# Kernel optimization log

Hardware: AMD Instinct MI355X
Metric: run time of the kernel (lower is better)

Reference implementation:

```python
import jax, jax.numpy as jnp
import numpy as np

N = 20000      # nodes
E = 100000     # edges
B = 128        # graphs in batch
F_IN = 14      # node feature dim
DIM = 64       # hidden dim
E_FEAT = 4     # edge feature dim
MLP_H = 128    # edge MLP hidden


def setup_inputs() -> dict:
    key = jax.random.key(0)
    ks = jax.random.split(key, 26)

    def rn(k, shape, fan_in):
        return jax.random.normal(k, shape, jnp.float32) / np.sqrt(fan_in)

    d = {}
    d['x'] = jax.random.normal(ks[0], (N, F_IN), jnp.float32)
    d['edge_attr'] = jax.random.uniform(ks[1], (E, E_FEAT), jnp.float32)
    d['edge_index'] = jax.random.randint(ks[2], (2, E), 0, N)
    d['batch'] = jnp.sort(jax.random.randint(ks[3], (N,), 0, B))
    # lin0
    d['lin0_w'] = rn(ks[4], (F_IN, DIM), F_IN)
    d['lin0_b'] = jnp.zeros((DIM,), jnp.float32)
    # edge MLP: Linear(4,128) -> ReLU -> Linear(128, dim*dim)
    d['mlp_w1'] = rn(ks[5], (E_FEAT, MLP_H), E_FEAT)
    d['mlp_b1'] = jnp.zeros((MLP_H,), jnp.float32)
    d['mlp_w2'] = rn(ks[6], (MLP_H, DIM * DIM), MLP_H) * 0.1
    d['mlp_b2'] = jnp.zeros((DIM * DIM,), jnp.float32)
    # NNConv root weight + bias
    d['conv_root'] = rn(ks[7], (DIM, DIM), DIM)
    d['conv_bias'] = jnp.zeros((DIM,), jnp.float32)
    # GRU (input dim DIM, hidden DIM), torch gate order r,z,n
    d['gru_wi'] = rn(ks[8], (DIM, 3 * DIM), DIM)
    d['gru_wh'] = rn(ks[9], (DIM, 3 * DIM), DIM)
    d['gru_bi'] = jnp.zeros((3 * DIM,), jnp.float32)
    d['gru_bh'] = jnp.zeros((3 * DIM,), jnp.float32)
    # Set2Set LSTM (input 2*DIM, hidden DIM), torch gate order i,f,g,o
    d['lstm_wi'] = rn(ks[10], (2 * DIM, 4 * DIM), 2 * DIM)
    d['lstm_wh'] = rn(ks[11], (DIM, 4 * DIM), DIM)
    d['lstm_bi'] = jnp.zeros((4 * DIM,), jnp.float32)
    d['lstm_bh'] = jnp.zeros((4 * DIM,), jnp.float32)
    # output head
    d['lin1_w'] = rn(ks[12], (2 * DIM, DIM), 2 * DIM)
    d['lin1_b'] = jnp.zeros((DIM,), jnp.float32)
    d['lin2_w'] = rn(ks[13], (DIM, 1), DIM)
    d['lin2_b'] = jnp.zeros((1,), jnp.float32)
    return d


def _forward(x, edge_attr, edge_index, batch,
             lin0_w, lin0_b, mlp_w1, mlp_b1, mlp_w2, mlp_b2,
             conv_root, conv_bias,
             gru_wi, gru_wh, gru_bi, gru_bh,
             lstm_wi, lstm_wh, lstm_bi, lstm_bh,
             lin1_w, lin1_b, lin2_w, lin2_b):
    src, dst = edge_index[0], edge_index[1]

    out = jax.nn.relu(x @ lin0_w + lin0_b)            # [N, DIM]
    h = out                                            # GRU hidden

    # per-edge weight matrices from edge MLP (shared across the 3 steps)
    ew = jax.nn.relu(edge_attr @ mlp_w1 + mlp_b1) @ mlp_w2 + mlp_b2
    ew = ew.reshape(E, DIM, DIM)                       # [E, DIM, DIM]
    # incoming-edge counts for scatter-mean
    cnt = jax.ops.segment_sum(jnp.ones((E,), jnp.float32), dst, num_segments=N)
    cnt = jnp.maximum(cnt, 1.0)[:, None]

    for _ in range(3):
        msg = jnp.einsum('ei,eio->eo', out[src], ew)   # gather + per-edge matmul
        agg = jax.ops.segment_sum(msg, dst, num_segments=N) / cnt
        m = jax.nn.relu(agg + out @ conv_root + conv_bias)
        # GRU cell (torch gate order: r, z, n)
        gi = m @ gru_wi + gru_bi
        gh = h @ gru_wh + gru_bh
        r = jax.nn.sigmoid(gi[:, :DIM] + gh[:, :DIM])
        z = jax.nn.sigmoid(gi[:, DIM:2 * DIM] + gh[:, DIM:2 * DIM])
        n = jnp.tanh(gi[:, 2 * DIM:] + r * gh[:, 2 * DIM:])
        h = (1.0 - z) * n + z * h
        out = h

    # Set2Set pooling, 3 processing steps
    q_star = jnp.zeros((B, 2 * DIM), jnp.float32)
    hl = jnp.zeros((B, DIM), jnp.float32)
    cl = jnp.zeros((B, DIM), jnp.float32)
    for _ in range(3):
        gates = q_star @ lstm_wi + hl @ lstm_wh + lstm_bi + lstm_bh  # [B, 4*DIM]
        i = jax.nn.sigmoid(gates[:, :DIM])
        f = jax.nn.sigmoid(gates[:, DIM:2 * DIM])
        g = jnp.tanh(gates[:, 2 * DIM:3 * DIM])
        o = jax.nn.sigmoid(gates[:, 3 * DIM:])
        cl = f * cl + i * g
        hl = o * jnp.tanh(cl)
        q = hl                                         # [B, DIM]
        e = jnp.sum(out * q[batch], axis=-1)           # [N]
        emax = jax.ops.segment_max(e, batch, num_segments=B)
        emax = jnp.where(jnp.isfinite(emax), emax, 0.0)
        a = jnp.exp(e - emax[batch])
        asum = jax.ops.segment_sum(a, batch, num_segments=B)
        a = a / jnp.maximum(asum, 1e-16)[batch]
        r_vec = jax.ops.segment_sum(a[:, None] * out, batch, num_segments=B)
        q_star = jnp.concatenate([q, r_vec], axis=-1)  # [B, 2*DIM]

    y = jax.nn.relu(q_star @ lin1_w + lin1_b) @ lin2_w + lin2_b
    return y.reshape(-1)                               # [B]


def reference(x, edge_attr, edge_index, batch,
              lin0_w, lin0_b, mlp_w1, mlp_b1, mlp_w2, mlp_b2,
              conv_root, conv_bias,
              gru_wi, gru_wh, gru_bi, gru_bh,
              lstm_wi, lstm_wh, lstm_bi, lstm_bh,
              lin1_w, lin1_b, lin2_w, lin2_b):
    return _forward(x, edge_attr, edge_index, batch,
                    lin0_w, lin0_b, mlp_w1, mlp_b1, mlp_w2, mlp_b2,
                    conv_root, conv_bias,
                    gru_wi, gru_wh, gru_bi, gru_bh,
                    lstm_wi, lstm_wh, lstm_bi, lstm_bh,
                    lin1_w, lin1_b, lin2_w, lin2_b)
```

## Files before the change

### kernel.cpp

```cpp
#include <hip/hip_runtime.h>
#include <math.h>

#define N_ 20000
#define E_ 100000
#define B_ 128
#define F_IN_ 14
#define DIM_ 64
#define E_FEAT_ 4
#define MLP_H_ 128
#define EWC_ 4096
#define PC_ 8192
#define PC2_ 8256

typedef __attribute__((ext_vector_type(4))) float f32x4;
typedef __attribute__((ext_vector_type(8))) _Float16 halfx8;

__global__ void lin0_kernel(const float* __restrict__ x, const float* __restrict__ w,
                            const float* __restrict__ b, float* __restrict__ out) {
    int idx = blockIdx.x * blockDim.x + threadIdx.x;
    if (idx >= N_ * DIM_) return;
    int n = idx >> 6, d = idx & 63;
    float acc = b[d];
#pragma unroll
    for (int f = 0; f < F_IN_; ++f) acc = fmaf(x[n * F_IN_ + f], w[f * DIM_ + d], acc);
    out[idx] = acc > 0.f ? acc : 0.f;
}

__global__ void deg_boff_kernel(const int* __restrict__ src, const int* __restrict__ dst,
                                float* __restrict__ cnt, int* __restrict__ cnt_src,
                                const int* __restrict__ batch, int* __restrict__ off_b) {
    int e = blockIdx.x * blockDim.x + threadIdx.x;
    if (e < E_) {
        atomicAdd(&cnt[dst[e]], 1.0f);
        atomicAdd(&cnt_src[src[e]], 1);
    }
    if (blockIdx.x == 0 && threadIdx.x <= B_) {
        int b = threadIdx.x;
        int lo = 0, hi = N_;
        while (lo < hi) {
            int mid = (lo + hi) >> 1;
            if (batch[mid] < b) lo = mid + 1; else hi = mid;
        }
        off_b[b] = lo;
    }
}

__global__ void scan_src(const int* __restrict__ cnt_src, int* __restrict__ src_off) {
    __shared__ int part[256];
    __shared__ int off[257];
    int t = threadIdx.x;
    const int per = (N_ + 255) / 256;
    int base = t * per;
    int s = 0;
    for (int i = 0; i < per; ++i) { int b = base + i; if (b < N_) s += cnt_src[b]; }
    part[t] = s;
    __syncthreads();
    if (t == 0) {
        int a = 0;
        for (int i = 0; i < 256; ++i) { off[i] = a; a += part[i]; }
        off[256] = a;
    }
    __syncthreads();
    int run = off[t];
    for (int i = 0; i < per; ++i) {
        int b = base + i;
        if (b < N_) { src_off[b] = run; run += cnt_src[b]; }
    }
    if (t == 0) src_off[N_] = off[256];
}

__global__ __launch_bounds__(256) void scatter_mlp1(
        const int* __restrict__ src, const int* __restrict__ dst,
        int* __restrict__ cur, const int* __restrict__ src_off,
        const float* __restrict__ ea, const float* __restrict__ w1,
        const float* __restrict__ b1, int* __restrict__ dsts,
        _Float16* __restrict__ h1s) {
    __shared__ float w1s[E_FEAT_ * MLP_H_];
    __shared__ float b1s[MLP_H_];
    int t = threadIdx.x;
    if (t < MLP_H_) b1s[t] = b1[t];
    for (int i = t; i < E_FEAT_ * MLP_H_; i += 256) w1s[i] = w1[i];
    __syncthreads();
    int e = blockIdx.x * 256 + t;
    if (e >= E_) return;
    int s = src[e];
    int p = src_off[s] + atomicAdd(&cur[s], 1);
    dsts[p] = dst[e];
    float a0 = ea[e * 4 + 0], a1 = ea[e * 4 + 1];
    float a2 = ea[e * 4 + 2], a3 = ea[e * 4 + 3];
    _Float16* hrow = h1s + (size_t)p * 128;
#pragma unroll
    for (int k8 = 0; k8 < 16; ++k8) {
        halfx8 v;
#pragma unroll
        for (int j = 0; j < 8; ++j) {
            int k = k8 * 8 + j;
            float acc = b1s[k];
            acc = fmaf(a0, w1s[k], acc);
            acc = fmaf(a1, w1s[128 + k], acc);
            acc = fmaf(a2, w1s[256 + k], acc);
            acc = fmaf(a3, w1s[384 + k], acc);
            v[j] = (_Float16)(acc > 0.f ? acc : 0.f);
        }
        *(halfx8*)&hrow[k8 * 8] = v;
    }
}

__global__ void prep_b(const float* __restrict__ w2, const float* __restrict__ b2,
                       _Float16* __restrict__ Bf) {
    int idx = blockIdx.x * blockDim.x + threadIdx.x;
    if (idx >= PC2_ * 64) return;
    int c16 = idx >> 10;
    int r   = idx & 1023;
    int ks  = r >> 9;
    int q   = (r >> 7) & 3;
    int lr  = (r >> 3) & 15;
    int j   = r & 7;
    int c = c16 * 16 + lr;
    int i = ks * 32 + q * 8 + j;
    float v;
    if (c < PC_) {
        int o = c >> 7, k = c & 127;
        v = w2[(size_t)k * EWC_ + i * 64 + o];
    } else {
        int o = c - PC_;
        v = b2[i * 64 + o];
    }
    Bf[idx] = (_Float16)v;
}

__global__ __launch_bounds__(512, 4) void fused_msg(
        const float* __restrict__ out, const _Float16* __restrict__ Bf,
        const _Float16* __restrict__ h1s,
        const int* __restrict__ dsts, const int* __restrict__ src_off,
        float* __restrict__ agg) {
    __shared__ _Float16 Plds[16 * 2048];
    const int tid = threadIdx.x;
    const int lane = tid & 63;
    const int w = __builtin_amdgcn_readfirstlane(tid >> 6);
    const int lrow = lane & 15, quad = lane >> 4;
    const int nb0 = blockIdx.x * 16;

    halfx8 aG[2];
    {
        const float* orow = out + (size_t)(nb0 + lrow) * 64 + quad * 8;
#pragma unroll
        for (int ks = 0; ks < 2; ++ks) {
            float4 v0 = *(const float4*)(orow + ks * 32);
            float4 v1 = *(const float4*)(orow + ks * 32 + 4);
            aG[ks][0] = (_Float16)v0.x; aG[ks][1] = (_Float16)v0.y;
            aG[ks][2] = (_Float16)v0.z; aG[ks][3] = (_Float16)v0.w;
            aG[ks][4] = (_Float16)v1.x; aG[ks][5] = (_Float16)v1.y;
            aG[ks][6] = (_Float16)v1.z; aG[ks][7] = (_Float16)v1.w;
        }
    }

    f32x4 qf[4];
#pragma unroll
    for (int f = 0; f < 4; ++f) {
        const _Float16* bc = &Bf[(size_t)(512 + f) * 1024 + quad * 128 + lrow * 8];
        halfx8 bq0 = *(const halfx8*)bc;
        halfx8 bq1 = *(const halfx8*)(bc + 512);
        f32x4 z = (f32x4){0.f, 0.f, 0.f, 0.f};
        z = __builtin_amdgcn_mfma_f32_16x16x32_f16(aG[0], bq0, z, 0, 0, 0);
        z = __builtin_amdgcn_mfma_f32_16x16x32_f16(aG[1], bq1, z, 0, 0, 0);
        qf[f] = z;
    }

    const int n0g = nb0 + 2 * w;
    const int beg0 = src_off[n0g];
    const int end0 = src_off[n0g + 1];
    const int end1 = src_off[n0g + 2];

#pragma unroll
    for (int p = 0; p < 4; ++p) {
        if (p) __syncthreads();

#pragma unroll 8
        for (int nf = 0; nf < 16; ++nf) {
            int cl = w * 256 + nf * 16 + lrow;
            size_t tb = (size_t)(p * 128 + w * 16 + nf) * 1024 + quad * 128 + lrow * 8;
            halfx8 b0 = *(const halfx8*)&Bf[tb];
            halfx8 b1 = *(const halfx8*)&Bf[tb + 512];
            f32x4 acc = (f32x4){0.f, 0.f, 0.f, 0.f};
            acc = __builtin_amdgcn_mfma_f32_16x16x32_f16(aG[0], b0, acc, 0, 0, 0);
            acc = __builtin_amdgcn_mfma_f32_16x16x32_f16(aG[1], b1, acc, 0, 0, 0);
            int o = cl >> 7, k = cl & 127;
            int kz = k ^ (quad << 5) ^ ((o & 7) << 3);
            int base = o * 2048 + kz;
#pragma unroll
            for (int rr = 0; rr < 4; ++rr)
                Plds[base + (quad * 4 + rr) * 128] = (_Float16)acc[rr];
        }
        __syncthreads();

        int o0 = p * 16;
#pragma unroll
        for (int nn = 0; nn < 2; ++nn) {
            int nl = 2 * w + nn;
            int beg = nn ? end0 : beg0;
            int endv = nn ? end1 : end0;
            if (beg == endv) continue;
            int srcl = ((nl >> 2) << 4) | lrow;
            int rsel = nl & 3;
            float qel = rsel == 0 ? qf[p][0] : rsel == 1 ? qf[p][1]
                      : rsel == 2 ? qf[p][2] : qf[p][3];
            float qv = __shfl(qel, srcl, 64);
            halfx8 bf[4];
#pragma unroll
            for (int ks = 0; ks < 4; ++ks) {
                int kk = (ks * 32 + quad * 8) ^ ((nl >> 2) << 5) ^ ((lrow & 7) << 3);
                bf[ks] = *(const halfx8*)&Plds[lrow * 2048 + nl * 128 + kk];
            }
            for (int g = beg; g < endv; g += 16) {
                int gcnt = endv - g; if (gcnt > 16) gcnt = 16;
                int ei = lrow < gcnt ? lrow : gcnt - 1;
                int gi = g + ei;
                int dv = dsts[gi];
                halfx8 af[4];
#pragma unroll
                for (int ks = 0; ks < 4; ++ks)
                    af[ks] = *(const halfx8*)&h1s[(size_t)gi * 128 + ks * 32 + quad * 8];
                f32x4 acc = (f32x4){0.f, 0.f, 0.f, 0.f};
#pragma unroll
                for (int ks = 0; ks < 4; ++ks)
                    acc = __builtin_amdgcn_mfma_f32_16x16x32_f16(
                        af[ks], bf[ks], acc, 0, 0, 0);
#pragma unroll
                for (int rr = 0; rr < 4; ++rr) {
                    int j = quad * 4 + rr;
                    int d = __shfl(dv, j, 64);
                    if (j < gcnt) {
                        atomicAdd(&agg[(size_t)d * 64 + o0 + lrow], acc[rr] + qv);
                    }
                }
            }
        }
    }
}

__global__ __launch_bounds__(256) void gru_kernel(float* __restrict__ out,
                                                  float* __restrict__ agg,
                                                  const float* __restrict__ cnt,
                                                  const float* __restrict__ root,
                                                  const float* __restrict__ cbias,
                                                  const float* __restrict__ wi,
                                                  const float* __restrict__ wh,
                                                  const float* __restrict__ bi,
                                                  const float* __restrict__ bh) {
    __shared__ float root_s[64 * 64];
    __shared__ float h_s[32 * 64];
    __shared__ float m_s[32 * 64];
    int tid = threadIdx.x;
    int lane = tid & 63;
    int wv = __builtin_amdgcn_readfirstlane(tid >> 6);
    int nb = blockIdx.x * 32;
#pragma unroll
    for (int it = 0; it < 4; ++it) {
        int i = it * 1024 + tid * 4;
        *(float4*)&root_s[i] = *(const float4*)&root[i];
    }
#pragma unroll
    for (int it = 0; it < 2; ++it) {
        int i = it * 1024 + tid * 4;
        *(float4*)&h_s[i] = *(const float4*)&out[(size_t)nb * 64 + i];
    }
    __syncthreads();

    int nbase = nb + wv * 8;
    float a[8];
#pragma unroll
    for (int j = 0; j < 8; ++j) {
        int n = nbase + j;
        float c = cnt[n]; c = c > 1.f ? c : 1.f;
        a[j] = agg[(size_t)n * 64 + lane] / c + cbias[lane];
        agg[(size_t)n * 64 + lane] = 0.f;
    }
    for (int i = 0; i < 64; ++i) {
        float rv = root_s[i * 64 + lane];
#pragma unroll
        for (int j = 0; j < 8; ++j)
            a[j] = fmaf(h_s[(wv * 8 + j) * 64 + i], rv, a[j]);
    }
#pragma unroll
    for (int j = 0; j < 8; ++j) {
        float m = a[j] > 0.f ? a[j] : 0.f;
        m_s[(wv * 8 + j) * 64 + lane] = m;
    }
    __syncthreads();

    float gir[8], giz[8], gin[8], ghr[8], ghz[8], ghn[8];
    float bi0 = bi[lane], bi1 = bi[64 + lane], bi2 = bi[128 + lane];
    float bh0 = bh[lane], bh1 = bh[64 + lane], bh2 = bh[128 + lane];
#pragma unroll
    for (int j = 0; j < 8; ++j) {
        gir[j] = bi0; giz[j] = bi1; gin[j] = bi2;
        ghr[j] = bh0; ghz[j] = bh1; ghn[j] = bh2;
    }
    for (int i = 0; i < 64; ++i) {
        float w0 = wi[i * 192 + lane];
        float w1 = wi[i * 192 + 64 + lane];
        float w2v = wi[i * 192 + 128 + lane];
        float u0 = wh[i * 192 + lane];
        float u1 = wh[i * 192 + 64 + lane];
        float u2 = wh[i * 192 + 128 + lane];
#pragma unroll
        for (int j = 0; j < 8; ++j) {
            float mi = m_s[(wv * 8 + j) * 64 + i];
            float hi = h_s[(wv * 8 + j) * 64 + i];
            gir[j] = fmaf(mi, w0, gir[j]);
            giz[j] = fmaf(mi, w1, giz[j]);
            gin[j] = fmaf(mi, w2v, gin[j]);
            ghr[j] = fmaf(hi, u0, ghr[j]);
            ghz[j] = fmaf(hi, u1, ghz[j]);
            ghn[j] = fmaf(hi, u2, ghn[j]);
        }
    }
#pragma unroll
    for (int j = 0; j < 8; ++j) {
        int n = nbase + j;
        float rg = 1.f / (1.f + expf(-(gir[j] + ghr[j])));
        float zg = 1.f / (1.f + expf(-(giz[j] + ghz[j])));
        float ng = tanhf(gin[j] + rg * ghn[j]);
        float h = h_s[(wv * 8 + j) * 64 + lane];
        out[(size_t)n * 64 + lane] = (1.f - zg) * ng + zg * h;
    }
}

__global__ __launch_bounds__(256) void lstm_all_kernel(
        const float* __restrict__ out, const int* __restrict__ off_b,
        float* __restrict__ e_ws,
        const float* __restrict__ wi, const float* __restrict__ wh,
        const float* __restrict__ bi, const float* __restrict__ bh,
        const float* __restrict__ hw1, const float* __restrict__ hb1,
        const float* __restrict__ hw2, const float* __restrict__ hb2,
        float* __restrict__ y) {
    int b = blockIdx.x;
    int t = threadIdx.x;
    __shared__ float qs[128], hs[64], cs[64], g[256];
    __shared__ float q[64];
    __shared__ float red[256], racc[256], sasum[4];

    if (t < 128) qs[t] = 0.f;
    if (t < 64) { hs[t] = 0.f; cs[t] = 0.f; }
    __syncthreads();

    int start = off_b[b], end = off_b[b + 1];

    for (int s = 0; s < 3; ++s) {
        {
            float acc = bi[t] + bh[t];
#pragma unroll 8
            for (int i = 0; i < 128; ++i) acc = fmaf(qs[i], wi[i * 256 + t], acc);
#pragma unroll 8
            for (int i = 0; i < 64; ++i) acc = fmaf(hs[i], wh[i * 256 + t], acc);
            g[t] = acc;
        }
        __syncthreads();
        if (t < 64) {
            float ig = 1.f / (1.f + expf(-g[t]));
            float fg = 1.f / (1.f + expf(-g[64 + t]));
            float gg = tanhf(g[128 + t]);
            float og = 1.f / (1.f + expf(-g[192 + t]));
            float c = fg * cs[t] + ig * gg;
            cs[t] = c;
            float h = og * tanhf(c);
            hs[t] = h;
            q[t] = h;
        }
        __syncthreads();

        float lmax = -1e30f;
        for (int n = start + t; n < end; n += 256) {
            float acc = 0.f;
#pragma unroll 16
            for (int d2 = 0; d2 < 64; ++d2) acc = fmaf(out[n * 64 + d2], q[d2], acc);
            e_ws[n] = acc;
            lmax = fmaxf(lmax, acc);
        }
        red[t] = lmax;
        __syncthreads();
        for (int s2 = 128; s2 > 0; s2 >>= 1) {
            if (t < s2) red[t] = fmaxf(red[t], red[t + s2]);
            __syncthreads();
        }
        float emax = red[0];
        int w = t >> 6, d = t & 63;
        float rl = 0.f, lasum = 0.f;
        for (int n = start + w; n < end; n += 4) {
            float a = expf(e_ws[n] - emax);
            rl = fmaf(a, out[n * 64 + d], rl);
            if (d == 0) lasum += a;
        }
        racc[t] = rl;
        if (d == 0) sasum[w] = lasum;
        __syncthreads();
        if (t < 64) {
            float r = racc[t] + racc[64 + t] + racc[128 + t] + racc[192 + t];
            float as = sasum[0] + sasum[1] + sasum[2] + sasum[3];
            as = fmaxf(as, 1e-16f);
            qs[t] = q[t];
            qs[64 + t] = r / as;
        }
        __syncthreads();
    }

    if (t < 64) {
        float acc = hb1[t];
#pragma unroll 8
        for (int i = 0; i < 128; ++i) acc = fmaf(qs[i], hw1[i * 64 + t], acc);
        acc = acc > 0.f ? acc : 0.f;
        float p = acc * hw2[t];
        for (int off = 32; off > 0; off >>= 1) p += __shfl_down(p, off, 64);
        if (t == 0) y[b] = p + hb2[0];
    }
}

extern "C" void kernel_launch(void* const* d_in, const int* in_sizes, int n_in,
                              void* d_out, int out_size, void* d_ws, size_t ws_size,
                              hipStream_t stream) {
    (void)in_sizes; (void)n_in; (void)out_size; (void)ws_size;
    const float* x        = (const float*)d_in[0];
    const float* ea       = (const float*)d_in[1];
    const int*   eidx     = (const int*)d_in[2];
    const int*   batch    = (const int*)d_in[3];
    const float* lin0_w   = (const float*)d_in[4];
    const float* lin0_b   = (const float*)d_in[5];
    const float* mlp_w1   = (const float*)d_in[6];
    const float* mlp_b1   = (const float*)d_in[7];
    const float* mlp_w2   = (const float*)d_in[8];
    const float* mlp_b2   = (const float*)d_in[9];
    const float* conv_root= (const float*)d_in[10];
    const float* conv_bias= (const float*)d_in[11];
    const float* gru_wi   = (const float*)d_in[12];
    const float* gru_wh   = (const float*)d_in[13];
    const float* gru_bi   = (const float*)d_in[14];
    const float* gru_bh   = (const float*)d_in[15];
    const float* lstm_wi  = (const float*)d_in[16];
    const float* lstm_wh  = (const float*)d_in[17];
    const float* lstm_bi  = (const float*)d_in[18];
    const float* lstm_bh  = (const float*)d_in[19];
    const float* lin1_w   = (const float*)d_in[20];
    const float* lin1_b   = (const float*)d_in[21];
    const float* lin2_w   = (const float*)d_in[22];
    const float* lin2_b   = (const float*)d_in[23];
    float* y = (float*)d_out;

    const int* src = eidx;
    const int* dst = eidx + E_;

    char* w = (char*)d_ws;
    auto carve = [&](size_t bytes) {
        char* p = w;
        w += (bytes + 255) & ~(size_t)255;
        return p;
    };
    float* out_buf = (float*)carve((size_t)N_ * DIM_ * 4);
    float* e_ws    = (float*)carve((size_t)N_ * 4);
    int*   off_b   = (int*)carve((size_t)(B_ + 1) * 4);
    _Float16* h1s  = (_Float16*)carve((size_t)E_ * MLP_H_ * 2);
    _Float16* Bf   = (_Float16*)carve((size_t)PC2_ * 64 * 2);
    int*   src_off = (int*)carve((size_t)(N_ + 1) * 4);
    int*   dsts    = (int*)carve((size_t)E_ * 4);
    char*  zero0   = w;
    float* agg     = (float*)carve((size_t)N_ * DIM_ * 4);
    float* cnt     = (float*)carve((size_t)N_ * 4);
    int*   cnt_src = (int*)carve((size_t)N_ * 4);
    int*   cur     = (int*)carve((size_t)N_ * 4);
    size_t zbytes  = (size_t)(w - zero0);

    hipMemsetAsync(zero0, 0, zbytes, stream);

    lin0_kernel<<<(N_ * DIM_ + 255) / 256, 256, 0, stream>>>(x, lin0_w, lin0_b, out_buf);
    deg_boff_kernel<<<(E_ + 255) / 256, 256, 0, stream>>>(src, dst, cnt, cnt_src,
                                                          batch, off_b);
    scan_src<<<1, 256, 0, stream>>>(cnt_src, src_off);
    scatter_mlp1<<<(E_ + 255) / 256, 256, 0, stream>>>(src, dst, cur, src_off,
                                                       ea, mlp_w1, mlp_b1,
                                                       dsts, h1s);
    prep_b<<<(PC2_ * 64 + 255) / 256, 256, 0, stream>>>(mlp_w2, mlp_b2, Bf);

    for (int step = 0; step < 3; ++step) {
        fused_msg<<<N_ / 16, 512, 0, stream>>>(out_buf, Bf, h1s, dsts,
                                               src_off, agg);
        gru_kernel<<<N_ / 32, 256, 0, stream>>>(out_buf, agg, cnt, conv_root, conv_bias,
                                                gru_wi, gru_wh, gru_bi, gru_bh);
    }

    lstm_all_kernel<<<B_, 256, 0, stream>>>(out_buf, off_b, e_ws,
                                            lstm_wi, lstm_wh, lstm_bi, lstm_bh,
                                            lin1_w, lin1_b, lin2_w, lin2_b, y);
}
```

Baseline: 582.8 us.

## Fuse setup kernels into one launch and widen GRU tile to 64 nodes

Merges lin0, degree/batch-offset, and prep_b weight packing into a single block-partitioned setup kernel, removing two launches. The GRU kernel now handles 64 nodes per block (16 per wave), so each weight value loaded from global memory is reused across more nodes. The input-gate and hidden-gate matmuls are split into separate loops to keep register pressure in check. This adds bounds checks for the partial last block, uses twice the LDS per block, and may lower occupancy and the number of blocks.

After: 614.3 us. +5.4%, slower.

```diff
diff --git a/kernel.cpp b/kernel.cpp
--- a/kernel.cpp
+++ b/kernel.cpp
@@ -12,36 +12,65 @@
 #define PC_ 8192
 #define PC2_ 8256
 
+#define LIN0_BLKS 5000
+#define DEG_BLKS 391
+#define PREPB_BLKS 2064
+
 typedef __attribute__((ext_vector_type(4))) float f32x4;
 typedef __attribute__((ext_vector_type(8))) _Float16 halfx8;
 
-__global__ void lin0_kernel(const float* __restrict__ x, const float* __restrict__ w,
-                            const float* __restrict__ b, float* __restrict__ out) {
-    int idx = blockIdx.x * blockDim.x + threadIdx.x;
-    if (idx >= N_ * DIM_) return;
-    int n = idx >> 6, d = idx & 63;
-    float acc = b[d];
-#pragma unroll
-    for (int f = 0; f < F_IN_; ++f) acc = fmaf(x[n * F_IN_ + f], w[f * DIM_ + d], acc);
-    out[idx] = acc > 0.f ? acc : 0.f;
-}
-
-__global__ void deg_boff_kernel(const int* __restrict__ src, const int* __restrict__ dst,
-                                float* __restrict__ cnt, int* __restrict__ cnt_src,
-                                const int* __restrict__ batch, int* __restrict__ off_b) {
-    int e = blockIdx.x * blockDim.x + threadIdx.x;
-    if (e < E_) {
-        atomicAdd(&cnt[dst[e]], 1.0f);
-        atomicAdd(&cnt_src[src[e]], 1);
-    }
-    if (blockIdx.x == 0 && threadIdx.x <= B_) {
-        int b = threadIdx.x;
-        int lo = 0, hi = N_;
-        while (lo < hi) {
-            int mid = (lo + hi) >> 1;
-            if (batch[mid] < b) lo = mid + 1; else hi = mid;
-        }
-        off_b[b] = lo;
+__global__ __launch_bounds__(256) void setup_a(
+        const float* __restrict__ x, const float* __restrict__ lw,
+        const float* __restrict__ lb, float* __restrict__ out,
+        const int* __restrict__ src, const int* __restrict__ dst,
+        float* __restrict__ cnt, int* __restrict__ cnt_src,
+        const int* __restrict__ batch, int* __restrict__ off_b,
+        const float* __restrict__ w2, const float* __restrict__ b2,
+        _Float16* __restrict__ Bf) {
+    int b = blockIdx.x;
+    int t = threadIdx.x;
+    if (b < LIN0_BLKS) {
+        int idx = b * 256 + t;
+        int n = idx >> 6, d = idx & 63;
+        float acc = lb[d];
+#pragma unroll
+        for (int f = 0; f < F_IN_; ++f) acc = fmaf(x[n * F_IN_ + f], lw[f * DIM_ + d], acc);
+        out[idx] = acc > 0.f ? acc : 0.f;
+    } else if (b < LIN0_BLKS + DEG_BLKS) {
+        int e = (b - LIN0_BLKS) * 256 + t;
+        if (e < E_) {
+            atomicAdd(&cnt[dst[e]], 1.0f);
+            atomicAdd(&cnt_src[src[e]], 1);
+        }
+        if (b == LIN0_BLKS && t <= B_) {
+            int bb = t;
+            int lo = 0, hi = N_;
+            while (lo < hi) {
+                int mid = (lo + hi) >> 1;
+                if (batch[mid] < bb) lo = mid + 1; else hi = mid;
+            }
+            off_b[bb] = lo;
+        }
+    } else {
+        int idx = (b - LIN0_BLKS - DEG_BLKS) * 256 + t;
+        if (idx >= PC2_ * 64) return;
+        int c16 = idx >> 10;
+        int r   = idx & 1023;
+        int ks  = r >> 9;
+        int q   = (r >> 7) & 3;
+        int lr  = (r >> 3) & 15;
+        int j   = r & 7;
+        int c = c16 * 16 + lr;
+        int i = ks * 32 + q * 8 + j;
+        float v;
+        if (c < PC_) {
+            int o = c >> 7, k = c & 127;
+            v = w2[(size_t)k * EWC_ + i * 64 + o];
+        } else {
+            int o = c - PC_;
+            v = b2[i * 64 + o];
+        }
+        Bf[idx] = (_Float16)v;
     }
 }
 
@@ -106,29 +135,6 @@
     }
 }
 
-__global__ void prep_b(const float* __restrict__ w2, const float* __restrict__ b2,
-                       _Float16* __restrict__ Bf) {
-    int idx = blockIdx.x * blockDim.x + threadIdx.x;
-    if (idx >= PC2_ * 64) return;
-    int c16 = idx >> 10;
-    int r   = idx & 1023;
-    int ks  = r >> 9;
-    int q   = (r >> 7) & 3;
-    int lr  = (r >> 3) & 15;
-    int j   = r & 7;
-    int c = c16 * 16 + lr;
-    int i = ks * 32 + q * 8 + j;
-    float v;
-    if (c < PC_) {
-        int o = c >> 7, k = c & 127;
-        v = w2[(size_t)k * EWC_ + i * 64 + o];
-    } else {
-        int o = c - PC_;
-        v = b2[i * 64 + o];
-    }
-    Bf[idx] = (_Float16)v;
-}
-
 __global__ __launch_bounds__(512, 4) void fused_msg(
         const float* __restrict__ out, const _Float16* __restrict__ Bf,
         const _Float16* __restrict__ h1s,
@@ -249,81 +255,97 @@
                                                   const float* __restrict__ bi,
                                                   const float* __restrict__ bh) {
     __shared__ float root_s[64 * 64];
-    __shared__ float h_s[32 * 64];
-    __shared__ float m_s[32 * 64];
+    __shared__ float h_s[64 * 64];
+    __shared__ float m_s[64 * 64];
     int tid = threadIdx.x;
     int lane = tid & 63;
     int wv = __builtin_amdgcn_readfirstlane(tid >> 6);
-    int nb = blockIdx.x * 32;
+    int nb = blockIdx.x * 64;
 #pragma unroll
     for (int it = 0; it < 4; ++it) {
         int i = it * 1024 + tid * 4;
         *(float4*)&root_s[i] = *(const float4*)&root[i];
     }
 #pragma unroll
-    for (int it = 0; it < 2; ++it) {
+    for (int it = 0; it < 4; ++it) {
         int i = it * 1024 + tid * 4;
-        *(float4*)&h_s[i] = *(const float4*)&out[(size_t)nb * 64 + i];
+        int gidx = nb * 64 + i;
+        float4 v = gidx < N_ * 64 ? *(const float4*)&out[gidx]
+                                  : (float4){0.f, 0.f, 0.f, 0.f};
+        *(float4*)&h_s[i] = v;
     }
     __syncthreads();
 
-    int nbase = nb + wv * 8;
-    float a[8];
-#pragma unroll
-    for (int j = 0; j < 8; ++j) {
+    int nbase = nb + wv * 16;
+    float a[16];
+#pragma unroll
+    for (int j = 0; j < 16; ++j) {
         int n = nbase + j;
-        float c = cnt[n]; c = c > 1.f ? c : 1.f;
-        a[j] = agg[(size_t)n * 64 + lane] / c + cbias[lane];
-        agg[(size_t)n * 64 + lane] = 0.f;
+        if (n < N_) {
+            float c = cnt[n]; c = c > 1.f ? c : 1.f;
+            a[j] = agg[(size_t)n * 64 + lane] / c + cbias[lane];
+            agg[(size_t)n * 64 + lane] = 0.f;
+        } else {
+            a[j] = 0.f;
+        }
     }
     for (int i = 0; i < 64; ++i) {
         float rv = root_s[i * 64 + lane];
 #pragma unroll
-        for (int j = 0; j < 8; ++j)
-            a[j] = fmaf(h_s[(wv * 8 + j) * 64 + i], rv, a[j]);
-    }
-#pragma unroll
-    for (int j = 0; j < 8; ++j) {
-        float m = a[j] > 0.f ? a[j] : 0.f;
-        m_s[(wv * 8 + j) * 64 + lane] = m;
-    }
+        for (int j = 0; j < 16; ++j)
+            a[j] = fmaf(h_s[(wv * 16 + j) * 64 + i], rv, a[j]);
+    }
+#pragma unroll
+    for (int j = 0; j < 16; ++j)
+        m_s[(wv * 16 + j) * 64 + lane] = a[j] > 0.f ? a[j] : 0.f;
     __syncthreads();
 
-    float gir[8], giz[8], gin[8], ghr[8], ghz[8], ghn[8];
-    float bi0 = bi[lane], bi1 = bi[64 + lane], bi2 = bi[128 + lane];
-    float bh0 = bh[lane], bh1 = bh[64 + lane], bh2 = bh[128 + lane];
-#pragma unroll
-    for (int j = 0; j < 8; ++j) {
-        gir[j] = bi0; giz[j] = bi1; gin[j] = bi2;
-        ghr[j] = bh0; ghz[j] = bh1; ghn[j] = bh2;
+    float gr[16], gz[16], gn[16];
+    {
+        float b0 = bi[lane], b1 = bi[64 + lane], b2v = bi[128 + lane];
+#pragma unroll
+        for (int j = 0; j < 16; ++j) { gr[j] = b0; gz[j] = b1; gn[j] = b2v; }
     }
     for (int i = 0; i < 64; ++i) {
         float w0 = wi[i * 192 + lane];
         float w1 = wi[i * 192 + 64 + lane];
         float w2v = wi[i * 192 + 128 + lane];
+#pragma unroll
+        for (int j = 0; j < 16; ++j) {
+            float mi = m_s[(wv * 16 + j) * 64 + i];
+            gr[j] = fmaf(mi, w0, gr[j]);
+            gz[j] = fmaf(mi, w1, gz[j]);
+            gn[j] = fmaf(mi, w2v, gn[j]);
+        }
+    }
+    float hr[16], hz[16], hn[16];
+    {
+        float b0 = bh[lane], b1 = bh[64 + lane], b2v = bh[128 + lane];
+#pragma unroll
+        for (int j = 0; j < 16; ++j) { hr[j] = b0; hz[j] = b1; hn[j] = b2v; }
+    }
+    for (int i = 0; i < 64; ++i) {
         float u0 = wh[i * 192 + lane];
         float u1 = wh[i * 192 + 64 + lane];
         float u2 = wh[i * 192 + 128 + lane];
 #pragma unroll
-        for (int j = 0; j < 8; ++j) {
-            float mi = m_s[(wv * 8 + j) * 64 + i];
-            float hi = h_s[(wv * 8 + j) * 64 + i];
-            gir[j] = fmaf(mi, w0, gir[j]);
-            giz[j] = fmaf(mi, w1, giz[j]);
-            gin[j] = fmaf(mi, w2v, gin[j]);
-            ghr[j] = fmaf(hi, u0, ghr[j]);
-            ghz[j] = fmaf(hi, u1, ghz[j]);
-            ghn[j] = fmaf(hi, u2, ghn[j]);
-        }
-    }
-#pragma unroll
-    for (int j = 0; j < 8; ++j) {
+        for (int j = 0; j < 16; ++j) {
+            float hi = h_s[(wv * 16 + j) * 64 + i];
+            hr[j] = fmaf(hi, u0, hr[j]);
+            hz[j] = fmaf(hi, u1, hz[j]);
+            hn[j] = fmaf(hi, u2, hn[j]);
+        }
+    }
+#pragma unroll
+    for (int j = 0; j < 16; ++j) {
         int n = nbase + j;
-        float rg = 1.f / (1.f + expf(-(gir[j] + ghr[j])));
-        float zg = 1.f / (1.f + expf(-(giz[j] + ghz[j])));
-        float ng = tanhf(gin[j] + rg * ghn[j]);
-        float h = h_s[(wv * 8 + j) * 64 + lane];
-        out[(size_t)n * 64 + lane] = (1.f - zg) * ng + zg * h;
+        if (n < N_) {
+            float rg = 1.f / (1.f + expf(-(gr[j] + hr[j])));
+            float zg = 1.f / (1.f + expf(-(gz[j] + hz[j])));
+            float ng = tanhf(gn[j] + rg * hn[j]);
+            float h = h_s[(wv * 16 + j) * 64 + lane];
+            out[(size_t)n * 64 + lane] = (1.f - zg) * ng + zg * h;
+        }
     }
 }
 
@@ -471,20 +493,21 @@
 
     hipMemsetAsync(zero0, 0, zbytes, stream);
 
-    lin0_kernel<<<(N_ * DIM_ + 255) / 256, 256, 0, stream>>>(x, lin0_w, lin0_b, out_buf);
-    deg_boff_kernel<<<(E_ + 255) / 256, 256, 0, stream>>>(src, dst, cnt, cnt_src,
-                                                          batch, off_b);
+    setup_a<<<LIN0_BLKS + DEG_BLKS + PREPB_BLKS, 256, 0, stream>>>(
+        x, lin0_w, lin0_b, out_buf, src, dst, cnt, cnt_src, batch, off_b,
+        mlp_w2, mlp_b2, Bf);
     scan_src<<<1, 256, 0, stream>>>(cnt_src, src_off);
     scatter_mlp1<<<(E_ + 255) / 256, 256, 0, stream>>>(src, dst, cur, src_off,
                                                        ea, mlp_w1, mlp_b1,
                                                        dsts, h1s);
-    prep_b<<<(PC2_ * 64 + 255) / 256, 256, 0, stream>>>(mlp_w2, mlp_b2, Bf);
 
     for (int step = 0; step < 3; ++step) {
         fused_msg<<<N_ / 16, 512, 0, stream>>>(out_buf, Bf, h1s, dsts,
                                                src_off, agg);
-        gru_kernel<<<N_ / 32, 256, 0, stream>>>(out_buf, agg, cnt, conv_root, conv_bias,
-                                                gru_wi, gru_wh, gru_bi, gru_bh);
+        gru_kernel<<<(N_ + 63) / 64, 256, 0, stream>>>(out_buf, agg, cnt,
+                                                       conv_root, conv_bias,
+                                                       gru_wi, gru_wh,
+                                                       gru_bi, gru_bh);
     }
 
     lstm_all_kernel<<<B_, 256, 0, stream>>>(out_buf, off_b, e_ws,
```
